# Performance work log

Hardware: AMD Instinct MI355X
Metric: run time of the kernel (lower is better)

The kernel has to match this reference:

```python
import jax, jax.numpy as jnp
import numpy as np

B, S, F = 64, 512, 1024
D_MODEL, D_MEM, D_IN, H, D_OUT, N_SYNC, T, H_NLM = 2048, 32, 1024, 16, 1000, 512, 16, 32
DH = D_IN // H


def _ln(x, g, b):
    m = x.mean(-1, keepdims=True)
    v = ((x - m) ** 2).mean(-1, keepdims=True)
    return (x - m) * jax.lax.rsqrt(v + 1e-5) * g + b


def setup_inputs() -> dict:
    key = jax.random.key(0)
    ks = jax.random.split(key, 24)
    def n(i, shape, fan):
        return jax.random.normal(ks[i], shape, jnp.float32) * (fan ** -0.5)
    u = 1.0 / np.sqrt(D_MODEL)
    uh = 1.0 / np.sqrt(D_MODEL + D_MEM)
    return dict(
        x=jax.random.normal(ks[0], (B, S, F), jnp.float32),
        W_kv=n(1, (F, D_IN), F), b_kv=jnp.zeros((D_IN,)),
        g_kv=jnp.ones((D_IN,)), be_kv=jnp.zeros((D_IN,)),
        W_q=n(2, (N_SYNC, D_IN), N_SYNC), b_q=jnp.zeros((D_IN,)),
        W_aq=n(3, (D_IN, D_IN), D_IN), b_aq=jnp.zeros((D_IN,)),
        W_ak=n(4, (D_IN, D_IN), D_IN), b_ak=jnp.zeros((D_IN,)),
        W_av=n(5, (D_IN, D_IN), D_IN), b_av=jnp.zeros((D_IN,)),
        W_ao=n(6, (D_IN, D_IN), D_IN), b_ao=jnp.zeros((D_IN,)),
        W_s1=n(7, (D_IN + D_MODEL, D_MODEL), D_IN + D_MODEL), b_s1=jnp.zeros((D_MODEL,)),
        W_s2=n(8, (D_MODEL, D_MODEL), D_MODEL), b_s2=jnp.zeros((D_MODEL,)),
        g_s=jnp.ones((D_MODEL,)), be_s=jnp.zeros((D_MODEL,)),
        W_n1=n(9, (D_MODEL, D_MEM, H_NLM), D_MEM), b_n1=jnp.zeros((D_MODEL, H_NLM)),
        W_n2=n(10, (D_MODEL, H_NLM), H_NLM), b_n2=jnp.zeros((D_MODEL,)),
        g_n=jnp.ones((D_MODEL,)), be_n=jnp.zeros((D_MODEL,)),
        init_state=jax.random.uniform(ks[11], (D_MODEL,), jnp.float32, -u, u),
        init_hist=jax.random.uniform(ks[12], (D_MODEL, D_MEM), jnp.float32, -uh, uh),
        decay_action=jax.random.uniform(ks[13], (N_SYNC,), jnp.float32, 0.0, 2.0),
        decay_out=jax.random.uniform(ks[14], (N_SYNC,), jnp.float32, 0.0, 2.0),
        W_out=n(15, (N_SYNC, D_OUT), N_SYNC), b_out=jnp.zeros((D_OUT,)),
        idx_la=jax.random.randint(ks[16], (N_SYNC,), 0, D_MODEL),
        idx_ra=jax.random.randint(ks[17], (N_SYNC,), 0, D_MODEL),
        idx_lo=jax.random.randint(ks[18], (N_SYNC,), 0, D_MODEL),
        idx_ro=jax.random.randint(ks[19], (N_SYNC,), 0, D_MODEL),
    )


def reference(x, W_kv, b_kv, g_kv, be_kv, W_q, b_q, W_aq, b_aq, W_ak, b_ak,
              W_av, b_av, W_ao, b_ao, W_s1, b_s1, W_s2, b_s2, g_s, be_s,
              W_n1, b_n1, W_n2, b_n2, g_n, be_n, init_state, init_hist,
              decay_action, decay_out, W_out, b_out,
              idx_la, idx_ra, idx_lo, idx_ro):
    # kv features: Linear + LayerNorm, fixed across ticks -> project k,v once
    kv = _ln(x @ W_kv + b_kv, g_kv, be_kv)                      # (B,S,D_IN)
    kh = (kv @ W_ak + b_ak).reshape(B, S, H, DH)
    vh = (kv @ W_av + b_av).reshape(B, S, H, DH)
    # learnable exponential decay r = exp(-clamp(p,0,15))
    rA = jnp.exp(-jnp.clip(decay_action, 0.0, 15.0))[None, :]
    rO = jnp.exp(-jnp.clip(decay_out, 0.0, 15.0))[None, :]
    act0 = jnp.broadcast_to(init_state, (B, D_MODEL))
    hist0 = jnp.broadcast_to(init_hist, (B, D_MODEL, D_MEM))
    # out-sync initialized before loop (None branch): alpha=prod, beta=1
    aO0 = act0[:, idx_lo] * act0[:, idx_ro]
    bO0 = jnp.ones_like(aO0)
    # action-sync None branch at tick0 == recurrence from alpha=beta=0
    aA0 = jnp.zeros((B, N_SYNC), x.dtype)
    bA0 = jnp.zeros((B, N_SYNC), x.dtype)

    def step(carry, _):
        act, hist, aA, bA, aO, bO = carry
        pA = act[:, idx_la] * act[:, idx_ra]                    # paired-neuron gather
        aA = rA * aA + pA
        bA = rA * bA + 1.0
        sync_a = aA * jax.lax.rsqrt(bA)
        q = sync_a @ W_q + b_q                                  # (B,D_IN)
        qh = (q @ W_aq + b_aq).reshape(B, H, DH)
        attn_w = jax.nn.softmax(jnp.einsum('bhd,bshd->bhs', qh, kh) / np.sqrt(DH), axis=-1)
        attn = jnp.einsum('bhs,bshd->bhd', attn_w, vh).reshape(B, D_IN) @ W_ao + b_ao
        pre = jnp.concatenate([attn, act], axis=-1)             # (B, D_IN+D_MODEL)
        pre_act = _ln(jax.nn.gelu(pre @ W_s1 + b_s1) @ W_s2 + b_s2, g_s, be_s)
        hist = jnp.concatenate([hist[:, :, 1:], pre_act[:, :, None]], axis=-1)
        # per-neuron deep NLM over the memory window
        hmid = jax.nn.relu(jnp.einsum('bdm,dmh->bdh', hist, W_n1) + b_n1)
        act = _ln(jnp.einsum('bdh,dh->bd', hmid, W_n2) + b_n2, g_n, be_n)
        pO = act[:, idx_lo] * act[:, idx_ro]
        aO = rO * aO + pO
        bO = rO * bO + 1.0
        pred = (aO * jax.lax.rsqrt(bO)) @ W_out + b_out         # (B,D_OUT)
        logp = jax.nn.log_softmax(pred, axis=-1)
        ne = -(jnp.exp(logp) * logp).sum(-1) / np.log(D_OUT)    # normalized entropy
        return (act, hist, aA, bA, aO, bO), (pred, ne)

    _, (preds, nes) = jax.lax.scan(step, (act0, hist0, aA0, bA0, aO0, bO0), None, length=T)
    predictions = jnp.transpose(preds, (1, 2, 0))               # (B,D_OUT,T)
    certainties = jnp.transpose(jnp.stack([nes, 1.0 - nes], axis=1), (2, 1, 0))  # (B,2,T)
    return predictions, certainties
```

## Files before the change

### kernel.cpp

```cpp
#include <hip/hip_runtime.h>
#include <hip/hip_bf16.h>


#define B_ 64
#define S_ 512
#define F_ 1024
#define DMODEL 2048
#define DMEM 32
#define DIN 1024
#define NH 16
#define DH 64
#define DOUT 1000
#define NSYNC 512
#define TICKS 16
#define HNLM 32
#define HIST_W 48

typedef __attribute__((ext_vector_type(8))) short short8;
typedef __attribute__((ext_vector_type(4))) float f32x4;

__device__ inline void store_f(float* p, float v) { *p = v; }
__device__ inline void store_f(__hip_bfloat16* p, float v) { *p = __float2bfloat16(v); }

__device__ inline short f2bs(float f) {
  __hip_bfloat16 h = __float2bfloat16(f);
  return *reinterpret_cast<short*>(&h);
}

__device__ inline float bfs(short x) {
  return __uint_as_float(((unsigned)(unsigned short)x) << 16);
}

__device__ inline float gelu_f(float x) {
  float x3 = x * x * x;
  return 0.5f * x * (1.f + tanhf(0.7978845608028654f * (x + 0.044715f * x3)));
}

__device__ inline float bf_lo(unsigned v) { return __uint_as_float(v << 16); }
__device__ inline float bf_hi(unsigned v) { return __uint_as_float(v & 0xffff0000u); }

__global__ __launch_bounds__(256) void transpose_bf16_kernel(const float* __restrict__ W,
                                                             __hip_bfloat16* __restrict__ Wt,
                                                             int K, int N, int Npad) {
  __shared__ float t[32][33];
  const int tx = threadIdx.x, ty = threadIdx.y;
  const int n0 = blockIdx.x * 32, k0 = blockIdx.y * 32;
#pragma unroll
  for (int i = 0; i < 4; i++) {
    int k = k0 + ty + i * 8;
    t[ty + i * 8][tx] = (k < K && n0 + tx < N) ? W[(size_t)k * N + n0 + tx] : 0.f;
  }
  __syncthreads();
#pragma unroll
  for (int i = 0; i < 4; i++) {
    int n = n0 + ty + i * 8;
    if (n < Npad && k0 + tx < K)
      Wt[(size_t)n * K + k0 + tx] = __float2bfloat16(t[tx][ty + i * 8]);
  }
}

__global__ void conv_bf16_kernel(const float* __restrict__ src, __hip_bfloat16* __restrict__ dst,
                                 int n) {
  int i = blockIdx.x * 256 + threadIdx.x;
  if (i < n) dst[i] = __float2bfloat16(src[i]);
}

__global__ void bqaq_kernel(const float* __restrict__ b_q, const float* __restrict__ b_aq,
                            const __hip_bfloat16* __restrict__ Wt_aq, float* __restrict__ b_qaq) {
  int n = blockIdx.x * 256 + threadIdx.x;
  if (n >= DIN) return;
  const __hip_bfloat16* wr = Wt_aq + (size_t)n * DIN;
  float s = b_aq[n];
  for (int k = 0; k < DIN; k++) s += b_q[k] * __bfloat162float(wr[k]);
  b_qaq[n] = s;
}

__device__ inline short8 load_chunk(const __hip_bfloat16* p) {
  return *reinterpret_cast<const short8*>(p);
}
__device__ inline short8 load_chunk(const float* p) {
  short8 r;
#pragma unroll
  for (int j = 0; j < 8; j++) r[j] = f2bs(p[j]);
  return r;
}

template <int TRANSC, typename TA, typename TC>
__global__ __launch_bounds__(256) void gemm_big(const TA* __restrict__ A,
                                                const __hip_bfloat16* __restrict__ Bt,
                                                const float* __restrict__ bias,
                                                TC* __restrict__ C, int M, int N, int K) {
  __shared__ short lsA[128 * 64];
  __shared__ short lsB[128 * 64];
  const int tid = threadIdx.x;
  const int l = tid & 63, w = tid >> 6;
  const int wr = (w >> 1) * 64, wc = (w & 1) * 64;
  const int nwg = gridDim.x * gridDim.y;
  const int flat = blockIdx.y * gridDim.x + blockIdx.x;
  const int wk = (flat & 7) * (nwg >> 3) + (flat >> 3);
  const int brow = (wk / gridDim.x) * 128, bcol = (wk % gridDim.x) * 128;
  f32x4 acc[4][4];
#pragma unroll
  for (int i = 0; i < 4; i++)
#pragma unroll
    for (int j = 0; j < 4; j++)
#pragma unroll
      for (int r = 0; r < 4; r++) acc[i][j][r] = 0.f;

  short8 ra[4], rb[4];
  auto gload = [&](int k0) {
#pragma unroll
    for (int q = 0; q < 4; q++) {
      int i = tid + q * 256;
      int row = i >> 3, c = i & 7;
      ra[q] = load_chunk(A + (size_t)(brow + row) * K + k0 + c * 8);
      rb[q] = load_chunk(Bt + (size_t)(bcol + row) * K + k0 + c * 8);
    }
  };
  auto lwrite = [&]() {
#pragma unroll
    for (int q = 0; q < 4; q++) {
      int i = tid + q * 256;
      int row = i >> 3, c = i & 7;
      int sw = c ^ (row & 7);
      *reinterpret_cast<short8*>(&lsA[row * 64 + sw * 8]) = ra[q];
      *reinterpret_cast<short8*>(&lsB[row * 64 + sw * 8]) = rb[q];
    }
  };
  gload(0);
  for (int k0 = 0; k0 < K; k0 += 64) {
    __syncthreads();
    lwrite();
    if (k0 + 64 < K) gload(k0 + 64);
    __syncthreads();
#pragma unroll
    for (int ks = 0; ks < 2; ks++) {
      short8 af[4], bfv[4];
#pragma unroll
      for (int mi = 0; mi < 4; mi++) {
        int row = wr + mi * 16 + (l & 15);
        int c = ks * 4 + (l >> 4);
        af[mi] = *reinterpret_cast<const short8*>(&lsA[row * 64 + (c ^ (row & 7)) * 8]);
      }
#pragma unroll
      for (int ni = 0; ni < 4; ni++) {
        int row = wc + ni * 16 + (l & 15);
        int c = ks * 4 + (l >> 4);
        bfv[ni] = *reinterpret_cast<const short8*>(&lsB[row * 64 + (c ^ (row & 7)) * 8]);
      }
#pragma unroll
      for (int mi = 0; mi < 4; mi++)
#pragma unroll
        for (int ni = 0; ni < 4; ni++)
          acc[mi][ni] =
              __builtin_amdgcn_mfma_f32_16x16x32_bf16(af[mi], bfv[ni], acc[mi][ni], 0, 0, 0);
    }
  }
#pragma unroll
  for (int mi = 0; mi < 4; mi++)
#pragma unroll
    for (int ni = 0; ni < 4; ni++)
#pragma unroll
      for (int r = 0; r < 4; r++) {
        int row = brow + wr + mi * 16 + (l >> 4) * 4 + r;
        int col = bcol + wc + ni * 16 + (l & 15);
        float v = acc[mi][ni][r];
        if (bias) v += bias[col];
        if (TRANSC == 1) {
          store_f(&C[(size_t)col * M + row], v);
        } else if (TRANSC == 2) {
          int bb = row >> 9, s = row & 511, hh = col >> 6, dd = col & 63;
          store_f(&C[(((size_t)(bb * 16 + hh) * 512) + s) * 64 + dd], v);
        } else {
          store_f(&C[(size_t)row * N + col], v);
        }
      }
}

template <typename TOUT>
__global__ __launch_bounds__(256) void ln_kernel(const float* __restrict__ x,
                                                 const float* __restrict__ g,
                                                 const float* __restrict__ be,
                                                 TOUT* __restrict__ out, int C,
                                                 size_t row_stride, int col_stride) {
  const int row = blockIdx.x;
  const int tid = threadIdx.x;
  const float* xr = x + (size_t)row * C;
  float s = 0.f, s2 = 0.f;
  for (int c = tid; c < C; c += 256) {
    float v = xr[c];
    s += v;
    s2 += v * v;
  }
  __shared__ float r1[256], r2[256];
  r1[tid] = s;
  r2[tid] = s2;
  __syncthreads();
  for (int st = 128; st > 0; st >>= 1) {
    if (tid < st) {
      r1[tid] += r1[tid + st];
      r2[tid] += r2[tid + st];
    }
    __syncthreads();
  }
  float mean = r1[0] / C;
  float var = r2[0] / C - mean * mean;
  float inv = 1.0f / sqrtf(var + 1e-5f);
  for (int c = tid; c < C; c += 256) {
    float v = (xr[c] - mean) * inv * g[c] + be[c];
    store_f(&out[(size_t)row * row_stride + (size_t)c * col_stride], v);
  }
}

__global__ void init_pre_kernel(const float* __restrict__ init_state,
                                __hip_bfloat16* __restrict__ pre) {
  int i = blockIdx.x * 256 + threadIdx.x;
  if (i >= B_ * DMODEL) return;
  int b = i >> 11, j = i & (DMODEL - 1);
  pre[(size_t)b * 3072 + DIN + j] = __float2bfloat16(init_state[j]);
}

__global__ void init_hist_kernel(const float* __restrict__ init_hist, float* __restrict__ hist) {
  int i = blockIdx.x * 256 + threadIdx.x;
  if (i >= B_ * DMODEL * DMEM) return;
  int m = i & (DMEM - 1);
  int bd = i >> 5;
  int d = bd & (DMODEL - 1);
  hist[(size_t)bd * HIST_W + m] = init_hist[d * DMEM + m];
}

__global__ void init_sync_kernel(const float* __restrict__ init_state,
                                 const float* __restrict__ decay_action,
                                 const float* __restrict__ decay_out,
                                 const int* __restrict__ la, const int* __restrict__ ra,
                                 const int* __restrict__ lo, const int* __restrict__ ro,
                                 float* __restrict__ aA, float* __restrict__ bA,
                                 float* __restrict__ aO, float* __restrict__ bO,
                                 __hip_bfloat16* __restrict__ syncA, float* __restrict__ rAv,
                                 float* __restrict__ rOv) {
  int i = blockIdx.x * 256 + threadIdx.x;
  if (i >= B_ * NSYNC) return;
  int j = i & (NSYNC - 1);
  if (i < NSYNC) {
    rAv[i] = expf(-fminf(fmaxf(decay_action[i], 0.f), 15.f));
    rOv[i] = expf(-fminf(fmaxf(decay_out[i], 0.f), 15.f));
  }
  float pA = init_state[la[j]] * init_state[ra[j]];
  aA[i] = pA;
  bA[i] = 1.f;
  syncA[i] = __float2bfloat16(pA);
  aO[i] = init_state[lo[j]] * init_state[ro[j]];
  bO[i] = 1.f;
}

template <typename EPI>
__device__ __forceinline__ void mm_tile64(const __hip_bfloat16* __restrict__ A, int lda,
                                          const __hip_bfloat16* __restrict__ Bt, int ldb,
                                          int bcol, int kb, int kchunk, int tid, short* lsA,
                                          short* lsB, EPI epi) {
  const int l = tid & 63, w = tid >> 6;
  f32x4 acc[4];
#pragma unroll
  for (int i = 0; i < 4; i++)
#pragma unroll
    for (int r = 0; r < 4; r++) acc[i][r] = 0.f;
  short8 ra[2], rb[2];
  auto gload = [&](int k0) {
#pragma unroll
    for (int q = 0; q < 2; q++) {
      int i = tid + q * 256;
      int row = i >> 3, c = i & 7;
      ra[q] = *reinterpret_cast<const short8*>(A + (size_t)row * lda + k0 + c * 8);
      rb[q] = *reinterpret_cast<const short8*>(Bt + (size_t)(bcol + row) * ldb + k0 + c * 8);
    }
  };
  auto lwrite = [&]() {
#pragma unroll
    for (int q = 0; q < 2; q++) {
      int i = tid + q * 256;
      int row = i >> 3, c = i & 7;
      int sw = c ^ (row & 7);
      *reinterpret_cast<short8*>(&lsA[row * 64 + sw * 8]) = ra[q];
      *reinterpret_cast<short8*>(&lsB[row * 64 + sw * 8]) = rb[q];
    }
  };
  gload(kb);
  for (int k0 = kb; k0 < kb + kchunk; k0 += 64) {
    __syncthreads();
    lwrite();
    if (k0 + 64 < kb + kchunk) gload(k0 + 64);
    __syncthreads();
#pragma unroll
    for (int ks = 0; ks < 2; ks++) {
      int rowa = w * 16 + (l & 15);
      int c = ks * 4 + (l >> 4);
      short8 af = *reinterpret_cast<const short8*>(&lsA[rowa * 64 + (c ^ (rowa & 7)) * 8]);
#pragma unroll
      for (int ni = 0; ni < 4; ni++) {
        int rowb = ni * 16 + (l & 15);
        short8 bfv = *reinterpret_cast<const short8*>(&lsB[rowb * 64 + (c ^ (rowb & 7)) * 8]);
        acc[ni] = __builtin_amdgcn_mfma_f32_16x16x32_bf16(af, bfv, acc[ni], 0, 0, 0);
      }
    }
  }
#pragma unroll
  for (int ni = 0; ni < 4; ni++)
#pragma unroll
    for (int r = 0; r < 4; r++) {
      int m = w * 16 + (l >> 4) * 4 + r;
      int n = bcol + ni * 16 + (l & 15);
      epi(m, n, acc[ni][r]);
    }
}

__global__ __launch_bounds__(256) void gemm_part(const __hip_bfloat16* __restrict__ A, int lda,
                                                 const __hip_bfloat16* __restrict__ Bt, int ldb,
                                                 float* __restrict__ part, int N, int kchunk) {
  __shared__ short lsA[64 * 64];
  __shared__ short lsB[64 * 64];
  const int tid = threadIdx.x;
  const int nt = blockIdx.x, ks = blockIdx.y;
  mm_tile64(A, lda, Bt, ldb, nt * 64, ks * kchunk, kchunk, tid, lsA, lsB,
            [&](int m, int n, float v) { part[((size_t)(ks * 64 + m)) * N + n] = v; });
}

__global__ void ao_red_kernel(const float* __restrict__ part, const float* __restrict__ bias,
                              __hip_bfloat16* __restrict__ pre, int KS) {
  int i = blockIdx.x * 256 + threadIdx.x;
  int m = i >> 10, n = i & 1023;
  float s = bias[n];
  for (int k = 0; k < KS; k++) s += part[((size_t)(k * 64 + m)) * DIN + n];
  pre[(size_t)m * 3072 + n] = __float2bfloat16(s);
}

__global__ void s1_red_kernel(const float* __restrict__ part, const float* __restrict__ bias,
                              __hip_bfloat16* __restrict__ h1, int KS) {
  int i = blockIdx.x * 256 + threadIdx.x;
  int m = i >> 11, n = i & 2047;
  float s = bias[n];
  for (int k = 0; k < KS; k++) s += part[((size_t)(k * 64 + m)) * DMODEL + n];
  h1[(size_t)m * DMODEL + n] = __float2bfloat16(gelu_f(s));
}

__global__ __launch_bounds__(256) void s2_red_ln_kernel(const float* __restrict__ part,
                                                        const float* __restrict__ bias,
                                                        const float* __restrict__ g,
                                                        const float* __restrict__ be,
                                                        float* __restrict__ hist, int KS, int t) {
  __shared__ float r1[256], r2[256];
  const int b = blockIdx.x;
  const int tid = threadIdx.x;
  float v8[8];
  float s = 0.f, s2 = 0.f;
#pragma unroll
  for (int i = 0; i < 8; i++) {
    int n = tid + i * 256;
    float x = bias[n];
    for (int k = 0; k < KS; k++) x += part[((size_t)(k * 64 + b)) * DMODEL + n];
    v8[i] = x;
    s += x;
    s2 += x * x;
  }
  r1[tid] = s;
  r2[tid] = s2;
  __syncthreads();
  for (int st = 128; st > 0; st >>= 1) {
    if (tid < st) {
      r1[tid] += r1[tid + st];
      r2[tid] += r2[tid + st];
    }
    __syncthreads();
  }
  float mean = r1[0] / DMODEL;
  float var = r2[0] / DMODEL - mean * mean;
  float inv = 1.f / sqrtf(var + 1e-5f);
#pragma unroll
  for (int i = 0; i < 8; i++) {
    int n = tid + i * 256;
    float pa = (v8[i] - mean) * inv * g[n] + be[n];
    hist[((size_t)b * DMODEL + n) * HIST_W + 32 + t] = pa;
  }
}

__global__ __launch_bounds__(256) void attn_kernel(const float* __restrict__ qpart,
                                                   const float* __restrict__ b_qaq,
                                                   const __hip_bfloat16* __restrict__ kh,
                                                   const __hip_bfloat16* __restrict__ vh,
                                                   __hip_bfloat16* __restrict__ attnv) {
  __shared__ float qs[64];
  __shared__ float wv[512];
  __shared__ float red[256];
  __shared__ float red2[2048];
  const int u = blockIdx.x;
  const int b = u >> 4, h = u & (NH - 1);
  const int tid = threadIdx.x;
  const __hip_bfloat16* Kp = kh + (size_t)u * (S_ * DH);
  const __hip_bfloat16* Vp = vh + (size_t)u * (S_ * DH);
  if (tid < DH) {
    int n = h * DH + tid;
    float s = b_qaq[n];
#pragma unroll
    for (int ks = 0; ks < 4; ks++) s += qpart[((size_t)(ks * 64 + b)) * DIN + n];
    qs[tid] = s;
  }
  __syncthreads();
  float sc[2];
#pragma unroll
  for (int r = 0; r < 2; ++r) {
    int s = tid + r * 256;
    const short8* kp = reinterpret_cast<const short8*>(Kp + (size_t)s * DH);
    float accv = 0.f;
#pragma unroll
    for (int q = 0; q < 8; ++q) {
      short8 kk = kp[q];
#pragma unroll
      for (int j = 0; j < 8; ++j) accv += qs[q * 8 + j] * bfs(kk[j]);
    }
    sc[r] = accv * 0.125f;
  }
  red[tid] = fmaxf(sc[0], sc[1]);
  __syncthreads();
  for (int st = 128; st > 0; st >>= 1) {
    if (tid < st) red[tid] = fmaxf(red[tid], red[tid + st]);
    __syncthreads();
  }
  const float mx = red[0];
  __syncthreads();
  float e0 = expf(sc[0] - mx), e1 = expf(sc[1] - mx);
  wv[tid] = e0;
  wv[tid + 256] = e1;
  red[tid] = e0 + e1;
  __syncthreads();
  for (int st = 128; st > 0; st >>= 1) {
    if (tid < st) red[tid] += red[tid + st];
    __syncthreads();
  }
  const float invZ = 1.f / red[0];
  __syncthreads();
  const int d8 = tid & 7, sg = tid >> 3;
  float pacc[8];
#pragma unroll
  for (int j = 0; j < 8; ++j) pacc[j] = 0.f;
  for (int s = sg; s < S_; s += 32) {
    float wgt = wv[s];
    short8 vvv = *reinterpret_cast<const short8*>(Vp + (size_t)s * DH + d8 * 8);
#pragma unroll
    for (int j = 0; j < 8; ++j) pacc[j] += wgt * bfs(vvv[j]);
  }
#pragma unroll
  for (int j = 0; j < 8; ++j) red2[sg * 64 + d8 * 8 + j] = pacc[j];
  __syncthreads();
  if (tid < DH) {
    float r = 0.f;
#pragma unroll
    for (int g2 = 0; g2 < 32; ++g2) r += red2[g2 * 64 + tid];
    attnv[b * DIN + h * DH + tid] = __float2bfloat16(r * invZ);
  }
}

__global__ __launch_bounds__(256) void nlm_kernel(const float* __restrict__ hist,
                                                  const float* __restrict__ W1,
                                                  const float* __restrict__ b1,
                                                  const float* __restrict__ W2,
                                                  const float* __restrict__ b2,
                                                  float* __restrict__ out, int t) {
  __shared__ float w1s[4096];
  __shared__ float b1s[128];
  const int tid = threadIdx.x;
  const int d0 = blockIdx.x * 4;
  for (int i = tid; i < 4096; i += 256) w1s[i] = W1[(size_t)d0 * 1024 + i];
  if (tid < 128) b1s[tid] = b1[d0 * 32 + tid];
  __syncthreads();
  const int b = tid & 63, dsub = tid >> 6;
  const int d = d0 + dsub;
  const float* hw = hist + ((size_t)(b * DMODEL + d)) * HIST_W + (t + 1);
  float win[DMEM];
#pragma unroll
  for (int m = 0; m < DMEM; ++m) win[m] = hw[m];
  const float* w1 = w1s + dsub * 1024;
  const float* bb = b1s + dsub * 32;
  const float* w2 = W2 + d * HNLM;
  float acc = 0.f;
  for (int h = 0; h < HNLM; ++h) {
    float s = bb[h];
#pragma unroll
    for (int m = 0; m < DMEM; ++m) s += win[m] * w1[m * HNLM + h];
    acc += fmaxf(s, 0.f) * w2[h];
  }
  out[(size_t)b * DMODEL + d] = acc + b2[d];
}

__global__ __launch_bounds__(256) void final_kernel(
    const float* __restrict__ nlmraw, const float* __restrict__ g_n,
    const float* __restrict__ be_n, const int* __restrict__ la, const int* __restrict__ ra,
    const int* __restrict__ lo, const int* __restrict__ ro, const float* __restrict__ rAv,
    const float* __restrict__ rOv, float* __restrict__ aA, float* __restrict__ bA,
    float* __restrict__ aO, float* __restrict__ bO, __hip_bfloat16* __restrict__ syncA,
    __hip_bfloat16* __restrict__ pre, const __hip_bfloat16* __restrict__ Wt_out,
    const float* __restrict__ b_out, float* __restrict__ outp, int t) {
  __shared__ float arow[2048];
  __shared__ float so[512];
  __shared__ float pv[1024];
  __shared__ float red[256], red2[256];
  const int b = blockIdx.x;
  const int tid = threadIdx.x;
  const float* xr = nlmraw + (size_t)b * DMODEL;
  float xv[8];
  float s = 0.f, s2 = 0.f;
#pragma unroll
  for (int i = 0; i < 8; i++) {
    float x = xr[tid + i * 256];
    xv[i] = x;
    s += x;
    s2 += x * x;
  }
  red[tid] = s;
  red2[tid] = s2;
  __syncthreads();
  for (int st = 128; st > 0; st >>= 1) {
    if (tid < st) {
      red[tid] += red[tid + st];
      red2[tid] += red2[tid + st];
    }
    __syncthreads();
  }
  float mean = red[0] / DMODEL;
  float var = red2[0] / DMODEL - mean * mean;
  float inv = 1.f / sqrtf(var + 1e-5f);
  __syncthreads();
#pragma unroll
  for (int i = 0; i < 8; i++) {
    int n = tid + i * 256;
    float av = (xv[i] - mean) * inv * g_n[n] + be_n[n];
    arow[n] = av;
    pre[(size_t)b * 3072 + DIN + n] = __float2bfloat16(av);
  }
  __syncthreads();
  for (int j = tid; j < NSYNC; j += 256) {
    size_t idx = (size_t)b * NSYNC + j;
    float pA = arow[la[j]] * arow[ra[j]];
    float r = rAv[j];
    float av2 = r * aA[idx] + pA, bv2 = r * bA[idx] + 1.f;
    aA[idx] = av2;
    bA[idx] = bv2;
    syncA[idx] = __float2bfloat16(av2 / sqrtf(bv2));
    float pO = arow[lo[j]] * arow[ro[j]];
    float ro2 = rOv[j];
    float av3 = ro2 * aO[idx] + pO, bv3 = ro2 * bO[idx] + 1.f;
    aO[idx] = av3;
    bO[idx] = bv3;
    so[j] = av3 / sqrtf(bv3);
  }
  __syncthreads();
  float pr[4];
#pragma unroll
  for (int i = 0; i < 4; i++) {
    int n = tid + i * 256;
    pr[i] = 0.f;
    if (n < DOUT) {
      const unsigned* wr = reinterpret_cast<const unsigned*>(Wt_out + (size_t)n * NSYNC);
      float sacc = b_out[n];
      for (int c = 0; c < 256; c++) {
        unsigned uu = wr[c];
        sacc += so[2 * c] * bf_lo(uu) + so[2 * c + 1] * bf_hi(uu);
      }
      pr[i] = sacc;
      pv[n] = sacc;
    }
  }
  __syncthreads();
  float m = -1e30f;
  for (int o = tid; o < DOUT; o += 256) m = fmaxf(m, pv[o]);
  red[tid] = m;
  __syncthreads();
  for (int st = 128; st > 0; st >>= 1) {
    if (tid < st) red[tid] = fmaxf(red[tid], red[tid + st]);
    __syncthreads();
  }
  m = red[0];
  __syncthreads();
  float z = 0.f, s1 = 0.f;
  for (int o = tid; o < DOUT; o += 256) {
    float wv2 = pv[o] - m;
    float e = expf(wv2);
    z += e;
    s1 += e * wv2;
  }
  red[tid] = z;
  __syncthreads();
  for (int st = 128; st > 0; st >>= 1) {
    if (tid < st) red[tid] += red[tid + st];
    __syncthreads();
  }
  const float Z = red[0];
  __syncthreads();
  red[tid] = s1;
  __syncthreads();
  for (int st = 128; st > 0; st >>= 1) {
    if (tid < st) red[tid] += red[tid + st];
    __syncthreads();
  }
  const float S1 = red[0];
  const float ne = -(S1 / Z - logf(Z)) / 6.907755278982137f;
#pragma unroll
  for (int i = 0; i < 4; i++) {
    int n = tid + i * 256;
    if (n < DOUT) outp[((size_t)b * DOUT + n) * TICKS + t] = pr[i];
  }
  if (tid == 0) {
    float* c = outp + (size_t)B_ * DOUT * TICKS;
    c[b * 2 * TICKS + t] = ne;
    c[b * 2 * TICKS + TICKS + t] = 1.f - ne;
  }
}

extern "C" void kernel_launch(void* const* d_in, const int* in_sizes, int n_in,
                              void* d_out, int out_size, void* d_ws, size_t ws_size,
                              hipStream_t stream) {
  const float* x = (const float*)d_in[0];
  const float* W_kv = (const float*)d_in[1];
  const float* b_kv = (const float*)d_in[2];
  const float* g_kv = (const float*)d_in[3];
  const float* be_kv = (const float*)d_in[4];
  const float* W_q = (const float*)d_in[5];
  const float* b_q = (const float*)d_in[6];
  const float* W_aq = (const float*)d_in[7];
  const float* b_aq = (const float*)d_in[8];
  const float* W_ak = (const float*)d_in[9];
  const float* b_ak = (const float*)d_in[10];
  const float* W_av = (const float*)d_in[11];
  const float* b_av = (const float*)d_in[12];
  const float* W_ao = (const float*)d_in[13];
  const float* b_ao = (const float*)d_in[14];
  const float* W_s1 = (const float*)d_in[15];
  const float* b_s1 = (const float*)d_in[16];
  const float* W_s2 = (const float*)d_in[17];
  const float* b_s2 = (const float*)d_in[18];
  const float* g_s = (const float*)d_in[19];
  const float* be_s = (const float*)d_in[20];
  const float* W_n1 = (const float*)d_in[21];
  const float* b_n1 = (const float*)d_in[22];
  const float* W_n2 = (const float*)d_in[23];
  const float* b_n2 = (const float*)d_in[24];
  const float* g_n = (const float*)d_in[25];
  const float* be_n = (const float*)d_in[26];
  const float* init_state = (const float*)d_in[27];
  const float* init_hist = (const float*)d_in[28];
  const float* decay_action = (const float*)d_in[29];
  const float* decay_out = (const float*)d_in[30];
  const float* W_out = (const float*)d_in[31];
  const float* b_out = (const float*)d_in[32];
  const int* idx_la = (const int*)d_in[33];
  const int* idx_ra = (const int*)d_in[34];
  const int* idx_lo = (const int*)d_in[35];
  const int* idx_ro = (const int*)d_in[36];
  float* out = (float*)d_out;

  char* wsb = (char*)d_ws;
  size_t off = 0;
  auto alloc = [&](size_t bytes) -> char* {
    char* p = wsb + off;
    off += (bytes + 255) & ~(size_t)255;
    return p;
  };
  const size_t MS = (size_t)B_ * S_;
  char* regionA = alloc(MS * DIN * 4);
  __hip_bfloat16* kv = (__hip_bfloat16*)alloc(MS * DIN * 2);
  float* histf = (float*)alloc((size_t)B_ * DMODEL * HIST_W * 4);
  __hip_bfloat16* Wt_kv = (__hip_bfloat16*)alloc((size_t)DIN * F_ * 2);
  __hip_bfloat16* Wt_ak = (__hip_bfloat16*)alloc((size_t)DIN * DIN * 2);
  __hip_bfloat16* Wt_av = (__hip_bfloat16*)alloc((size_t)DIN * DIN * 2);
  __hip_bfloat16* Wt_aq = (__hip_bfloat16*)alloc((size_t)DIN * DIN * 2);
  __hip_bfloat16* Wt_ao = (__hip_bfloat16*)alloc((size_t)DIN * DIN * 2);
  __hip_bfloat16* W_qb = (__hip_bfloat16*)alloc((size_t)NSYNC * DIN * 2);
  __hip_bfloat16* Wt_qaq = (__hip_bfloat16*)alloc((size_t)DIN * NSYNC * 2);
  __hip_bfloat16* Wt_s1 = (__hip_bfloat16*)alloc((size_t)DMODEL * (DIN + DMODEL) * 2);
  __hip_bfloat16* Wt_s2 = (__hip_bfloat16*)alloc((size_t)DMODEL * DMODEL * 2);
  __hip_bfloat16* Wt_out = (__hip_bfloat16*)alloc((size_t)DOUT * NSYNC * 2);
  float* b_qaq = (float*)alloc(DIN * 4);
  float* partial = (float*)alloc((size_t)8 * 64 * DMODEL * 4);
  float* aA = (float*)alloc((size_t)B_ * NSYNC * 4);
  float* bA = (float*)alloc((size_t)B_ * NSYNC * 4);
  float* aO = (float*)alloc((size_t)B_ * NSYNC * 4);
  float* bO = (float*)alloc((size_t)B_ * NSYNC * 4);
  __hip_bfloat16* syncA = (__hip_bfloat16*)alloc((size_t)B_ * NSYNC * 2);
  __hip_bfloat16* attnv = (__hip_bfloat16*)alloc((size_t)B_ * DIN * 2);
  __hip_bfloat16* pre = (__hip_bfloat16*)alloc((size_t)B_ * (DIN + DMODEL) * 2);
  __hip_bfloat16* h1 = (__hip_bfloat16*)alloc((size_t)B_ * DMODEL * 2);
  float* nlmraw = (float*)alloc((size_t)B_ * DMODEL * 4);
  float* rAv = (float*)alloc(NSYNC * 4);
  float* rOv = (float*)alloc(NSYNC * 4);

  float* kvraw = (float*)regionA;
  __hip_bfloat16* kh = (__hip_bfloat16*)regionA;
  __hip_bfloat16* vh = (__hip_bfloat16*)(regionA + MS * DIN * 2);

  dim3 t32x8(32, 8);
  transpose_bf16_kernel<<<dim3(F_ / 32, DIN / 32), t32x8, 0, stream>>>(W_kv, Wt_kv, F_, DIN, DIN);
  transpose_bf16_kernel<<<dim3(DIN / 32, DIN / 32), t32x8, 0, stream>>>(W_ak, Wt_ak, DIN, DIN, DIN);
  transpose_bf16_kernel<<<dim3(DIN / 32, DIN / 32), t32x8, 0, stream>>>(W_av, Wt_av, DIN, DIN, DIN);
  transpose_bf16_kernel<<<dim3(DIN / 32, DIN / 32), t32x8, 0, stream>>>(W_aq, Wt_aq, DIN, DIN, DIN);
  transpose_bf16_kernel<<<dim3(DIN / 32, DIN / 32), t32x8, 0, stream>>>(W_ao, Wt_ao, DIN, DIN, DIN);
  transpose_bf16_kernel<<<dim3(DMODEL / 32, (DIN + DMODEL) / 32), t32x8, 0, stream>>>(
      W_s1, Wt_s1, DIN + DMODEL, DMODEL, DMODEL);
  transpose_bf16_kernel<<<dim3(DMODEL / 32, DMODEL / 32), t32x8, 0, stream>>>(W_s2, Wt_s2, DMODEL,
                                                                              DMODEL, DMODEL);
  transpose_bf16_kernel<<<dim3((DOUT + 31) / 32, NSYNC / 32), t32x8, 0, stream>>>(
      W_out, Wt_out, NSYNC, DOUT, DOUT);
  conv_bf16_kernel<<<(NSYNC * DIN + 255) / 256, 256, 0, stream>>>(W_q, W_qb, NSYNC * DIN);
  bqaq_kernel<<<4, 256, 0, stream>>>(b_q, b_aq, Wt_aq, b_qaq);

  gemm_big<0, float, float><<<dim3(DIN / 128, MS / 128), 256, 0, stream>>>(x, Wt_kv, b_kv, kvraw,
                                                                           (int)MS, DIN, F_);
  ln_kernel<__hip_bfloat16><<<(int)MS, 256, 0, stream>>>(kvraw, g_kv, be_kv, kv, DIN, DIN, 1);
  gemm_big<2, __hip_bfloat16, __hip_bfloat16><<<dim3(DIN / 128, MS / 128), 256, 0, stream>>>(
      kv, Wt_ak, b_ak, kh, (int)MS, DIN, DIN);
  gemm_big<2, __hip_bfloat16, __hip_bfloat16><<<dim3(DIN / 128, MS / 128), 256, 0, stream>>>(
      kv, Wt_av, b_av, vh, (int)MS, DIN, DIN);
  gemm_big<1, __hip_bfloat16, __hip_bfloat16><<<dim3(DIN / 128, NSYNC / 128), 256, 0, stream>>>(
      W_qb, Wt_aq, nullptr, Wt_qaq, NSYNC, DIN, DIN);

  init_pre_kernel<<<(B_ * DMODEL + 255) / 256, 256, 0, stream>>>(init_state, pre);
  init_hist_kernel<<<(B_ * DMODEL * DMEM + 255) / 256, 256, 0, stream>>>(init_hist, histf);
  init_sync_kernel<<<(B_ * NSYNC + 255) / 256, 256, 0, stream>>>(
      init_state, decay_action, decay_out, idx_la, idx_ra, idx_lo, idx_ro, aA, bA, aO, bO, syncA,
      rAv, rOv);

  for (int t = 0; t < TICKS; ++t) {
    gemm_part<<<dim3(16, 4), 256, 0, stream>>>(syncA, NSYNC, Wt_qaq, NSYNC, partial, DIN, 128);
    attn_kernel<<<B_ * NH, 256, 0, stream>>>(partial, b_qaq, kh, vh, attnv);
    gemm_part<<<dim3(16, 8), 256, 0, stream>>>(attnv, DIN, Wt_ao, DIN, partial, DIN, 128);
    ao_red_kernel<<<256, 256, 0, stream>>>(partial, b_ao, pre, 8);
    gemm_part<<<dim3(32, 8), 256, 0, stream>>>(pre, DIN + DMODEL, Wt_s1, DIN + DMODEL, partial,
                                               DMODEL, 384);
    s1_red_kernel<<<512, 256, 0, stream>>>(partial, b_s1, h1, 8);
    gemm_part<<<dim3(32, 8), 256, 0, stream>>>(h1, DMODEL, Wt_s2, DMODEL, partial, DMODEL, 256);
    s2_red_ln_kernel<<<B_, 256, 0, stream>>>(partial, b_s2, g_s, be_s, histf, 8, t);
    nlm_kernel<<<DMODEL / 4, 256, 0, stream>>>(histf, W_n1, b_n1, W_n2, b_n2, nlmraw, t);
    final_kernel<<<B_, 256, 0, stream>>>(nlmraw, g_n, be_n, idx_la, idx_ra, idx_lo, idx_ro, rAv,
                                         rOv, aA, bA, aO, bO, syncA, pre, Wt_out, b_out, out, t);
  }
  (void)in_sizes; (void)n_in; (void)out_size; (void)ws_size;
}
```

Measured before the change: 2.679 ms.

## Fold W_ao into W_s1 and fuse query projection into final kernel

Precomputes W_ao·W_s1[:DIN] (and the matching bias) once, so each tick's attention output feeds the s1 GEMM directly and the ao GEMM and its reduction kernel are dropped. The per-tick query projection (syncA·Wt_qaq) moves into the tail of final_kernel as a per-batch matvec, which removes the separate gemm_part launch and the partial reduction inside attn. This cuts the per-tick kernel count from 10 to 7. In exchange it adds a serial 1024x512 matvec per block in final_kernel running on only 64 blocks, and the folded weight is rounded to bf16 a second time, which shifts numerics slightly.

```diff
diff --git a/kernel.cpp b/kernel.cpp
--- a/kernel.cpp
+++ b/kernel.cpp
@@ -41,7 +41,8 @@
 
 __global__ __launch_bounds__(256) void transpose_bf16_kernel(const float* __restrict__ W,
                                                              __hip_bfloat16* __restrict__ Wt,
-                                                             int K, int N, int Npad) {
+                                                             int K, int N, int Npad, int ldw,
+                                                             int koff) {
   __shared__ float t[32][33];
   const int tx = threadIdx.x, ty = threadIdx.y;
   const int n0 = blockIdx.x * 32, k0 = blockIdx.y * 32;
@@ -55,7 +56,7 @@
   for (int i = 0; i < 4; i++) {
     int n = n0 + ty + i * 8;
     if (n < Npad && k0 + tx < K)
-      Wt[(size_t)n * K + k0 + tx] = __float2bfloat16(t[tx][ty + i * 8]);
+      Wt[(size_t)n * ldw + koff + k0 + tx] = __float2bfloat16(t[tx][ty + i * 8]);
   }
 }
 
@@ -73,6 +74,15 @@
   float s = b_aq[n];
   for (int k = 0; k < DIN; k++) s += b_q[k] * __bfloat162float(wr[k]);
   b_qaq[n] = s;
+}
+
+__global__ void bs1c_kernel(const float* __restrict__ b_s1, const float* __restrict__ b_ao,
+                            const float* __restrict__ W_s1, float* __restrict__ b_s1c) {
+  int n = blockIdx.x * 256 + threadIdx.x;
+  if (n >= DMODEL) return;
+  float s = b_s1[n];
+  for (int k = 0; k < DIN; k++) s += b_ao[k] * W_s1[(size_t)k * DMODEL + n];
+  b_s1c[n] = s;
 }
 
 __device__ inline short8 load_chunk(const __hip_bfloat16* p) {
@@ -236,7 +246,7 @@
                                  const int* __restrict__ lo, const int* __restrict__ ro,
                                  float* __restrict__ aA, float* __restrict__ bA,
                                  float* __restrict__ aO, float* __restrict__ bO,
-                                 __hip_bfloat16* __restrict__ syncA, float* __restrict__ rAv,
+                                 float* __restrict__ syncA0, float* __restrict__ rAv,
                                  float* __restrict__ rOv) {
   int i = blockIdx.x * 256 + threadIdx.x;
   if (i >= B_ * NSYNC) return;
@@ -248,9 +258,32 @@
   float pA = init_state[la[j]] * init_state[ra[j]];
   aA[i] = pA;
   bA[i] = 1.f;
-  syncA[i] = __float2bfloat16(pA);
+  syncA0[i] = pA;
   aO[i] = init_state[lo[j]] * init_state[ro[j]];
   bO[i] = 1.f;
+}
+
+__global__ __launch_bounds__(256) void qh0_kernel(const float* __restrict__ syncA0,
+                                                  const __hip_bfloat16* __restrict__ Wt_qaq,
+                                                  const float* __restrict__ b_qaq,
+                                                  float* __restrict__ qhb) {
+  __shared__ float sa[512];
+  const int b = blockIdx.x;
+  const int tid = threadIdx.x;
+  sa[tid] = syncA0[(size_t)b * NSYNC + tid];
+  sa[tid + 256] = syncA0[(size_t)b * NSYNC + 256 + tid];
+  __syncthreads();
+#pragma unroll
+  for (int i = 0; i < 4; i++) {
+    int n = tid + i * 256;
+    const unsigned* wr = reinterpret_cast<const unsigned*>(Wt_qaq + (size_t)n * NSYNC);
+    float s = b_qaq[n];
+    for (int c = 0; c < 256; c++) {
+      unsigned uu = wr[c];
+      s += sa[2 * c] * bf_lo(uu) + sa[2 * c + 1] * bf_hi(uu);
+    }
+    qhb[(size_t)b * DIN + n] = s;
+  }
 }
 
 template <typename EPI>
@@ -322,15 +355,6 @@
   const int nt = blockIdx.x, ks = blockIdx.y;
   mm_tile64(A, lda, Bt, ldb, nt * 64, ks * kchunk, kchunk, tid, lsA, lsB,
             [&](int m, int n, float v) { part[((size_t)(ks * 64 + m)) * N + n] = v; });
-}
-
-__global__ void ao_red_kernel(const float* __restrict__ part, const float* __restrict__ bias,
-                              __hip_bfloat16* __restrict__ pre, int KS) {
-  int i = blockIdx.x * 256 + threadIdx.x;
-  int m = i >> 10, n = i & 1023;
-  float s = bias[n];
-  for (int k = 0; k < KS; k++) s += part[((size_t)(k * 64 + m)) * DIN + n];
-  pre[(size_t)m * 3072 + n] = __float2bfloat16(s);
 }
 
 __global__ void s1_red_kernel(const float* __restrict__ part, const float* __restrict__ bias,
@@ -382,11 +406,10 @@
   }
 }
 
-__global__ __launch_bounds__(256) void attn_kernel(const float* __restrict__ qpart,
-                                                   const float* __restrict__ b_qaq,
+__global__ __launch_bounds__(256) void attn_kernel(const float* __restrict__ qhb,
                                                    const __hip_bfloat16* __restrict__ kh,
                                                    const __hip_bfloat16* __restrict__ vh,
-                                                   __hip_bfloat16* __restrict__ attnv) {
+                                                   __hip_bfloat16* __restrict__ pre) {
   __shared__ float qs[64];
   __shared__ float wv[512];
   __shared__ float red[256];
@@ -396,13 +419,7 @@
   const int tid = threadIdx.x;
   const __hip_bfloat16* Kp = kh + (size_t)u * (S_ * DH);
   const __hip_bfloat16* Vp = vh + (size_t)u * (S_ * DH);
-  if (tid < DH) {
-    int n = h * DH + tid;
-    float s = b_qaq[n];
-#pragma unroll
-    for (int ks = 0; ks < 4; ks++) s += qpart[((size_t)(ks * 64 + b)) * DIN + n];
-    qs[tid] = s;
-  }
+  if (tid < DH) qs[tid] = qhb[(size_t)b * DIN + h * DH + tid];
   __syncthreads();
   float sc[2];
 #pragma unroll
@@ -454,7 +471,7 @@
     float r = 0.f;
 #pragma unroll
     for (int g2 = 0; g2 < 32; ++g2) r += red2[g2 * 64 + tid];
-    attnv[b * DIN + h * DH + tid] = __float2bfloat16(r * invZ);
+    pre[(size_t)b * 3072 + h * DH + tid] = __float2bfloat16(r * invZ);
   }
 }
 
@@ -495,10 +512,12 @@
     const float* __restrict__ be_n, const int* __restrict__ la, const int* __restrict__ ra,
     const int* __restrict__ lo, const int* __restrict__ ro, const float* __restrict__ rAv,
     const float* __restrict__ rOv, float* __restrict__ aA, float* __restrict__ bA,
-    float* __restrict__ aO, float* __restrict__ bO, __hip_bfloat16* __restrict__ syncA,
-    __hip_bfloat16* __restrict__ pre, const __hip_bfloat16* __restrict__ Wt_out,
+    float* __restrict__ aO, float* __restrict__ bO, __hip_bfloat16* __restrict__ pre,
+    const __hip_bfloat16* __restrict__ Wt_qaq, const float* __restrict__ b_qaq,
+    float* __restrict__ qhb, const __hip_bfloat16* __restrict__ Wt_out,
     const float* __restrict__ b_out, float* __restrict__ outp, int t) {
   __shared__ float arow[2048];
+  __shared__ float sa[512];
   __shared__ float so[512];
   __shared__ float pv[1024];
   __shared__ float red[256], red2[256];
@@ -543,7 +562,7 @@
     float av2 = r * aA[idx] + pA, bv2 = r * bA[idx] + 1.f;
     aA[idx] = av2;
     bA[idx] = bv2;
-    syncA[idx] = __float2bfloat16(av2 / sqrtf(bv2));
+    sa[j] = av2 / sqrtf(bv2);
     float pO = arow[lo[j]] * arow[ro[j]];
     float ro2 = rOv[j];
     float av3 = ro2 * aO[idx] + pO, bv3 = ro2 * bO[idx] + 1.f;
@@ -552,6 +571,17 @@
     so[j] = av3 / sqrtf(bv3);
   }
   __syncthreads();
+#pragma unroll
+  for (int i = 0; i < 4; i++) {
+    int n = tid + i * 256;
+    const unsigned* wr = reinterpret_cast<const unsigned*>(Wt_qaq + (size_t)n * NSYNC);
+    float sacc = b_qaq[n];
+    for (int c = 0; c < 256; c++) {
+      unsigned uu = wr[c];
+      sacc += sa[2 * c] * bf_lo(uu) + sa[2 * c + 1] * bf_hi(uu);
+    }
+    qhb[(size_t)b * DIN + n] = sacc;
+  }
   float pr[4];
 #pragma unroll
   for (int i = 0; i < 4; i++) {
@@ -671,20 +701,22 @@
   __hip_bfloat16* Wt_ak = (__hip_bfloat16*)alloc((size_t)DIN * DIN * 2);
   __hip_bfloat16* Wt_av = (__hip_bfloat16*)alloc((size_t)DIN * DIN * 2);
   __hip_bfloat16* Wt_aq = (__hip_bfloat16*)alloc((size_t)DIN * DIN * 2);
-  __hip_bfloat16* Wt_ao = (__hip_bfloat16*)alloc((size_t)DIN * DIN * 2);
+  __hip_bfloat16* W_ao_b = (__hip_bfloat16*)alloc((size_t)DIN * DIN * 2);
   __hip_bfloat16* W_qb = (__hip_bfloat16*)alloc((size_t)NSYNC * DIN * 2);
   __hip_bfloat16* Wt_qaq = (__hip_bfloat16*)alloc((size_t)DIN * NSYNC * 2);
-  __hip_bfloat16* Wt_s1 = (__hip_bfloat16*)alloc((size_t)DMODEL * (DIN + DMODEL) * 2);
+  __hip_bfloat16* Wts1top = (__hip_bfloat16*)alloc((size_t)DMODEL * DIN * 2);
+  __hip_bfloat16* Wt_s1c = (__hip_bfloat16*)alloc((size_t)DMODEL * (DIN + DMODEL) * 2);
   __hip_bfloat16* Wt_s2 = (__hip_bfloat16*)alloc((size_t)DMODEL * DMODEL * 2);
   __hip_bfloat16* Wt_out = (__hip_bfloat16*)alloc((size_t)DOUT * NSYNC * 2);
   float* b_qaq = (float*)alloc(DIN * 4);
+  float* b_s1c = (float*)alloc(DMODEL * 4);
   float* partial = (float*)alloc((size_t)8 * 64 * DMODEL * 4);
   float* aA = (float*)alloc((size_t)B_ * NSYNC * 4);
   float* bA = (float*)alloc((size_t)B_ * NSYNC * 4);
   float* aO = (float*)alloc((size_t)B_ * NSYNC * 4);
   float* bO = (float*)alloc((size_t)B_ * NSYNC * 4);
-  __hip_bfloat16* syncA = (__hip_bfloat16*)alloc((size_t)B_ * NSYNC * 2);
-  __hip_bfloat16* attnv = (__hip_bfloat16*)alloc((size_t)B_ * DIN * 2);
+  float* syncA0 = (float*)alloc((size_t)B_ * NSYNC * 4);
+  float* qhb = (float*)alloc((size_t)B_ * DIN * 4);
   __hip_bfloat16* pre = (__hip_bfloat16*)alloc((size_t)B_ * (DIN + DMODEL) * 2);
   __hip_bfloat16* h1 = (__hip_bfloat16*)alloc((size_t)B_ * DMODEL * 2);
   float* nlmraw = (float*)alloc((size_t)B_ * DMODEL * 4);
@@ -696,19 +728,27 @@
   __hip_bfloat16* vh = (__hip_bfloat16*)(regionA + MS * DIN * 2);
 
   dim3 t32x8(32, 8);
-  transpose_bf16_kernel<<<dim3(F_ / 32, DIN / 32), t32x8, 0, stream>>>(W_kv, Wt_kv, F_, DIN, DIN);
-  transpose_bf16_kernel<<<dim3(DIN / 32, DIN / 32), t32x8, 0, stream>>>(W_ak, Wt_ak, DIN, DIN, DIN);
-  transpose_bf16_kernel<<<dim3(DIN / 32, DIN / 32), t32x8, 0, stream>>>(W_av, Wt_av, DIN, DIN, DIN);
-  transpose_bf16_kernel<<<dim3(DIN / 32, DIN / 32), t32x8, 0, stream>>>(W_aq, Wt_aq, DIN, DIN, DIN);
-  transpose_bf16_kernel<<<dim3(DIN / 32, DIN / 32), t32x8, 0, stream>>>(W_ao, Wt_ao, DIN, DIN, DIN);
-  transpose_bf16_kernel<<<dim3(DMODEL / 32, (DIN + DMODEL) / 32), t32x8, 0, stream>>>(
-      W_s1, Wt_s1, DIN + DMODEL, DMODEL, DMODEL);
+  transpose_bf16_kernel<<<dim3(F_ / 32, DIN / 32), t32x8, 0, stream>>>(W_kv, Wt_kv, F_, DIN, DIN,
+                                                                       F_, 0);
+  transpose_bf16_kernel<<<dim3(DIN / 32, DIN / 32), t32x8, 0, stream>>>(W_ak, Wt_ak, DIN, DIN,
+                                                                        DIN, DIN, 0);
+  transpose_bf16_kernel<<<dim3(DIN / 32, DIN / 32), t32x8, 0, stream>>>(W_av, Wt_av, DIN, DIN,
+                                                                        DIN, DIN, 0);
+  transpose_bf16_kernel<<<dim3(DIN / 32, DIN / 32), t32x8, 0, stream>>>(W_aq, Wt_aq, DIN, DIN,
+                                                                        DIN, DIN, 0);
+  transpose_bf16_kernel<<<dim3(DMODEL / 32, DIN / 32), t32x8, 0, stream>>>(W_s1, Wts1top, DIN,
+                                                                           DMODEL, DMODEL, DIN, 0);
+  transpose_bf16_kernel<<<dim3(DMODEL / 32, DMODEL / 32), t32x8, 0, stream>>>(
+      W_s1 + (size_t)DIN * DMODEL, Wt_s1c, DMODEL, DMODEL, DMODEL, DIN + DMODEL, DIN);
   transpose_bf16_kernel<<<dim3(DMODEL / 32, DMODEL / 32), t32x8, 0, stream>>>(W_s2, Wt_s2, DMODEL,
-                                                                              DMODEL, DMODEL);
+                                                                              DMODEL, DMODEL,
+                                                                              DMODEL, 0);
   transpose_bf16_kernel<<<dim3((DOUT + 31) / 32, NSYNC / 32), t32x8, 0, stream>>>(
-      W_out, Wt_out, NSYNC, DOUT, DOUT);
+      W_out, Wt_out, NSYNC, DOUT, DOUT, NSYNC, 0);
   conv_bf16_kernel<<<(NSYNC * DIN + 255) / 256, 256, 0, stream>>>(W_q, W_qb, NSYNC * DIN);
+  conv_bf16_kernel<<<(DIN * DIN + 255) / 256, 256, 0, stream>>>(W_ao, W_ao_b, DIN * DIN);
   bqaq_kernel<<<4, 256, 0, stream>>>(b_q, b_aq, Wt_aq, b_qaq);
+  bs1c_kernel<<<8, 256, 0, stream>>>(b_s1, b_ao, W_s1, b_s1c);
 
   gemm_big<0, float, float><<<dim3(DIN / 128, MS / 128), 256, 0, stream>>>(x, Wt_kv, b_kv, kvraw,
                                                                            (int)MS, DIN, F_);
@@ -719,26 +759,27 @@
       kv, Wt_av, b_av, vh, (int)MS, DIN, DIN);
   gemm_big<1, __hip_bfloat16, __hip_bfloat16><<<dim3(DIN / 128, NSYNC / 128), 256, 0, stream>>>(
       W_qb, Wt_aq, nullptr, Wt_qaq, NSYNC, DIN, DIN);
+  gemm_big<1, __hip_bfloat16, __hip_bfloat16><<<dim3(DMODEL / 128, DIN / 128), 256, 0, stream>>>(
+      W_ao_b, Wts1top, nullptr, Wt_s1c, DIN + DMODEL, DMODEL, DIN);
 
   init_pre_kernel<<<(B_ * DMODEL + 255) / 256, 256, 0, stream>>>(init_state, pre);
   init_hist_kernel<<<(B_ * DMODEL * DMEM + 255) / 256, 256, 0, stream>>>(init_hist, histf);
   init_sync_kernel<<<(B_ * NSYNC + 255) / 256, 256, 0, stream>>>(
-      init_state, decay_action, decay_out, idx_la, idx_ra, idx_lo, idx_ro, aA, bA, aO, bO, syncA,
-      rAv, rOv);
+      init_state, decay_action, decay_out, idx_la, idx_ra, idx_lo, idx_ro, aA, bA, aO, bO,
+      syncA0, rAv, rOv);
+  qh0_kernel<<<B_, 256, 0, stream>>>(syncA0, Wt_qaq, b_qaq, qhb);
 
   for (int t = 0; t < TICKS; ++t) {
-    gemm_part<<<dim3(16, 4), 256, 0, stream>>>(syncA, NSYNC, Wt_qaq, NSYNC, partial, DIN, 128);
-    attn_kernel<<<B_ * NH, 256, 0, stream>>>(partial, b_qaq, kh, vh, attnv);
-    gemm_part<<<dim3(16, 8), 256, 0, stream>>>(attnv, DIN, Wt_ao, DIN, partial, DIN, 128);
-    ao_red_kernel<<<256, 256, 0, stream>>>(partial, b_ao, pre, 8);
-    gemm_part<<<dim3(32, 8), 256, 0, stream>>>(pre, DIN + DMODEL, Wt_s1, DIN + DMODEL, partial,
+    attn_kernel<<<B_ * NH, 256, 0, stream>>>(qhb, kh, vh, pre);
+    gemm_part<<<dim3(32, 8), 256, 0, stream>>>(pre, DIN + DMODEL, Wt_s1c, DIN + DMODEL, partial,
                                                DMODEL, 384);
-    s1_red_kernel<<<512, 256, 0, stream>>>(partial, b_s1, h1, 8);
+    s1_red_kernel<<<512, 256, 0, stream>>>(partial, b_s1c, h1, 8);
     gemm_part<<<dim3(32, 8), 256, 0, stream>>>(h1, DMODEL, Wt_s2, DMODEL, partial, DMODEL, 256);
     s2_red_ln_kernel<<<B_, 256, 0, stream>>>(partial, b_s2, g_s, be_s, histf, 8, t);
     nlm_kernel<<<DMODEL / 4, 256, 0, stream>>>(histf, W_n1, b_n1, W_n2, b_n2, nlmraw, t);
     final_kernel<<<B_, 256, 0, stream>>>(nlmraw, g_n, be_n, idx_la, idx_ra, idx_lo, idx_ro, rAv,
-                                         rOv, aA, bA, aO, bO, syncA, pre, Wt_out, b_out, out, t);
+                                         rOv, aA, bA, aO, bO, pre, Wt_qaq, b_qaq, qhb, Wt_out,
+                                         b_out, out, t);
   }
   (void)in_sizes; (void)n_in; (void)out_size; (void)ws_size;
 }
```

Result: slower. 3.191 ms (+19.1%).
